# Optimization experiments

Measured on AMD Instinct MI355X. Metric: run time of the kernel, lower is better.

## Reference

```python
import jax, jax.numpy as jnp
import numpy as np

TEMP = 1.0

def setup_inputs() -> dict:
    key = jax.random.key(0)
    k1, k2 = jax.random.split(key)
    B, T, C, Vp1 = 16, 2048, 256, 1025
    z = jax.random.normal(k1, (B, T, C), dtype=jnp.float32)
    mask = jnp.ones((B, T, 1), dtype=jnp.float32)
    codebook_weight = jax.random.normal(k2, (Vp1, C), dtype=jnp.float32)
    return {"z": z, "mask": mask, "codebook_weight": codebook_weight}

def reference(z, mask, codebook_weight):
    # e = codebook.embedding.weight.clone().detach()[1:, :]
    e = jax.lax.stop_gradient(codebook_weight[1:, :])  # [V, C]
    b, t, c = z.shape
    V = e.shape[0]
    z_flat = z.reshape(-1, c)                          # [N, C], N = b*t
    # sim(): cosine-sim matmul + log_softmax + argmax one-hot quantize
    cos_sim = jnp.matmul(z_flat, e.T)                  # [N, V]
    log_probs = jax.nn.log_softmax(cos_sim / TEMP, axis=1)
    indices = jnp.argmax(log_probs, axis=1)            # [N]
    # one_hot @ e is exactly a row gather -- avoid materializing one_hot
    z_q = e[indices]                                   # [N, C]
    z_q3 = z_q.reshape(b, t, c)
    # loss(): masked commitment + smoothness
    valid_count = mask.sum() * c
    commitment_loss = (jnp.square(z - jax.lax.stop_gradient(z_q3)) * mask).sum() / valid_count
    smoothness_loss = (jnp.square(z[:, :-1, :] - z[:, 1:, :]) * mask[:, 1:, :]).sum() / valid_count
    # codebook_usage(): (one_hot * mask).sum(0) / mask.sum(), normalized
    mflat = mask.reshape(-1)                           # [N]
    prob = jax.ops.segment_sum(mflat, indices, num_segments=V) / mflat.sum()
    e_mean = prob / prob.sum()
    return (smoothness_loss, commitment_loss, log_probs.reshape(b, t, V), z_q3, e_mean)
```

## Files before the change

kernel.cpp:

```cpp
#include <hip/hip_runtime.h>
#include <hip/hip_bf16.h>

#define TPB 1024
#define BM 32
#define NROW 32768
#define NBLK (NROW / BM)
#define VV 1024
#define KD 256
#define TT 2048

#define LP_OFF 2L
#define ZQ_OFF (2L + 33554432L)
#define EM_OFF (33554434L + 8388608L)

#define WS_HIST 0
#define WS_CSUM 1024
#define WS_SSUM 2048
#define WS_MSUM 3072
#define WS_E8 4096
#define WS_NEED (4096 * 4 + 32 * 1024 * 8 * 2)

typedef __attribute__((ext_vector_type(8))) short bf16x8;
typedef __attribute__((ext_vector_type(4))) float f32x4;

__device__ __forceinline__ void gl_lds16(const float* g, float* l) {
  __builtin_amdgcn_global_load_lds(
      (const __attribute__((address_space(1))) void*)g,
      (__attribute__((address_space(3))) void*)l, 16, 0, 0);
}

__device__ __forceinline__ unsigned short f2bf(float x) {
  unsigned u = __float_as_uint(x);
  unsigned r = ((u >> 16) & 1u) + 0x7FFFu;
  return (unsigned short)((u + r) >> 16);
}

__device__ __forceinline__ unsigned foldf(float v) {
  unsigned b = __float_as_uint(v);
  return b ^ ((unsigned)((int)b >> 31) | 0x80000000u);
}
__device__ __forceinline__ float unfoldf(unsigned k) {
  unsigned s = (unsigned)((int)k >> 31);
  return __uint_as_float(k ^ (0x80000000u | (~s & 0x7FFFFFFFu)));
}

__global__ __launch_bounds__(256) void tok_prep(
    const float* __restrict__ cw, unsigned short* __restrict__ e8) {
  int t = blockIdx.x * 256 + threadIdx.x;
  int o = t >> 10, n = t & 1023;
  const float* src = cw + (size_t)(1 + n) * KD + (o << 3);
  float4 a = *(const float4*)src;
  float4 b = *(const float4*)(src + 4);
  int4 pk;
  pk.x = f2bf(a.x) | ((unsigned)f2bf(a.y) << 16);
  pk.y = f2bf(a.z) | ((unsigned)f2bf(a.w) << 16);
  pk.z = f2bf(b.x) | ((unsigned)f2bf(b.y) << 16);
  pk.w = f2bf(b.z) | ((unsigned)f2bf(b.w) << 16);
  int U = ((n >> 6) << 11) + ((o >> 2) << 8) + (((n >> 4) & 3) << 6) +
          ((o & 3) << 4) + (n & 15);
  *(int4*)(e8 + ((size_t)U << 3)) = pk;
}

__global__ __launch_bounds__(TPB, 4) void tok_mfma(
    const float* __restrict__ z, const float* __restrict__ mask,
    const float* __restrict__ cw, const unsigned short* __restrict__ e8,
    float* __restrict__ out, float* __restrict__ ws) {
  __shared__ __align__(16) float z_s[BM][260];
  __shared__ __align__(16) unsigned short z8u[8192];
  __shared__ unsigned wkey[16][2][33];
  __shared__ float wsum_s[16][33];
  __shared__ float Mrow_s[32], lse_s[32];
  __shared__ float exv_s[32][4];
  __shared__ int exi_s[32][4];
  __shared__ int argi[32];
  __shared__ float mask_s[32];
  __shared__ float cred[16], sred[16];

  const int tid = threadIdx.x;
  const int lane = tid & 63;
  const int w = tid >> 6;
  const int g = lane >> 4;
  const int lm = lane & 15;
  const int c0 = w << 6;
  const int n0 = blockIdx.x * BM;

  gl_lds16(&z[(size_t)(n0 + w) * KD + (lane << 2)], &z_s[w][0]);
  gl_lds16(&z[(size_t)(n0 + 16 + w) * KD + (lane << 2)], &z_s[16 + w][0]);
  if (tid < 32) mask_s[tid] = mask[n0 + tid];
  __syncthreads();

  {
    int r = tid >> 5, o = tid & 31;
    float4 a = *(const float4*)&z_s[r][o << 3];
    float4 b = *(const float4*)&z_s[r][(o << 3) + 4];
    int4 pk;
    pk.x = f2bf(a.x) | ((unsigned)f2bf(a.y) << 16);
    pk.y = f2bf(a.z) | ((unsigned)f2bf(a.w) << 16);
    pk.z = f2bf(b.x) | ((unsigned)f2bf(b.y) << 16);
    pk.w = f2bf(b.z) | ((unsigned)f2bf(b.w) << 16);
    *(int4*)&z8u[(unsigned)(((o << 5) + (r ^ ((o & 7) << 2))) << 3)] = pk;
  }
  __syncthreads();

  const bf16x8* za = (const bf16x8*)z8u;
  const bf16x8* bb = (const bf16x8*)e8 + (w << 11) + (g << 4) + lm;
  f32x4 accA[4], accB[4];
  const f32x4 zz = {0.f, 0.f, 0.f, 0.f};
#pragma unroll
  for (int nt = 0; nt < 4; ++nt) { accA[nt] = zz; accB[nt] = zz; }
  bf16x8 bA[4], bB[4], bC[4];
#pragma unroll
  for (int nt = 0; nt < 4; ++nt) bA[nt] = bb[nt << 6];
#pragma unroll
  for (int nt = 0; nt < 4; ++nt) bB[nt] = bb[256 + (nt << 6)];
#pragma unroll
  for (int step = 0; step < 8; ++step) {
    if (step < 6) {
#pragma unroll
      for (int nt = 0; nt < 4; ++nt) bC[nt] = bb[((step + 2) << 8) + (nt << 6)];
    }
    const int oct = (step << 2) + g;
    const int sw = (oct & 7) << 2;
    bf16x8 a0 = za[(oct << 5) + (lm ^ sw)];
    bf16x8 a1 = za[(oct << 5) + ((16 + lm) ^ sw)];
#pragma unroll
    for (int nt = 0; nt < 4; ++nt) {
      accA[nt] = __builtin_amdgcn_mfma_f32_16x16x32_bf16(a0, bA[nt], accA[nt], 0, 0, 0);
      accB[nt] = __builtin_amdgcn_mfma_f32_16x16x32_bf16(a1, bA[nt], accB[nt], 0, 0, 0);
    }
#pragma unroll
    for (int nt = 0; nt < 4; ++nt) { bA[nt] = bB[nt]; bB[nt] = bC[nt]; }
  }

  unsigned colpack[4];
#pragma unroll
  for (int nt = 0; nt < 4; ++nt)
    colpack[nt] = 1023u - (unsigned)(c0 + (nt << 4) + lm);

  auto phase1 = [&](f32x4(&ac)[4], int mt) {
#pragma unroll
    for (int j = 0; j < 4; ++j) {
      int r = (mt << 4) + (g << 2) + j;
      unsigned cur[4];
#pragma unroll
      for (int nt = 0; nt < 4; ++nt)
        cur[nt] = (foldf(ac[nt][j]) & 0xFFFFFC00u) | colpack[nt];
      unsigned k1 = cur[0];
#pragma unroll
      for (int nt = 1; nt < 4; ++nt) k1 = k1 > cur[nt] ? k1 : cur[nt];
#pragma unroll
      for (int d = 1; d <= 8; d <<= 1) {
        unsigned o2 = __shfl_xor(k1, d);
        k1 = k1 > o2 ? k1 : o2;
      }
#pragma unroll
      for (int nt = 0; nt < 4; ++nt)
        if (cur[nt] == k1) cur[nt] = 0u;
      unsigned k2 = cur[0];
#pragma unroll
      for (int nt = 1; nt < 4; ++nt) k2 = k2 > cur[nt] ? k2 : cur[nt];
#pragma unroll
      for (int d = 1; d <= 8; d <<= 1) {
        unsigned o2 = __shfl_xor(k2, d);
        k2 = k2 > o2 ? k2 : o2;
      }
      if (lm == 0) {
        wkey[w][0][r] = k1;
        wkey[w][1][r] = k2;
      }
    }
  };
  phase1(accA, 0);
  phase1(accB, 1);
  __syncthreads();

  if (tid < 32) {
    int r = tid;
    unsigned mk = wkey[0][0][r];
#pragma unroll
    for (int w2 = 1; w2 < 16; ++w2) {
      unsigned k = wkey[w2][0][r];
      mk = mk > k ? mk : k;
    }
    Mrow_s[r] = unfoldf(mk & 0xFFFFFC00u);
  }
  __syncthreads();

  auto phase2 = [&](f32x4(&ac)[4], int mt) {
#pragma unroll
    for (int j = 0; j < 4; ++j) {
      int r = (mt << 4) + (g << 2) + j;
      float M = Mrow_s[r];
      float s = 0.f;
#pragma unroll
      for (int nt = 0; nt < 4; ++nt) s += __expf(ac[nt][j] - M);
#pragma unroll
      for (int d = 1; d <= 8; d <<= 1) s += __shfl_xor(s, d);
      if (lm == 0) wsum_s[w][r] = s;
    }
  };
  phase2(accA, 0);
  phase2(accB, 1);
  __syncthreads();

  if (tid < 32) {
    int r = tid;
    float S = 0.f;
#pragma unroll
    for (int w2 = 0; w2 < 16; ++w2) S += wsum_s[w2][r];
    lse_s[r] = Mrow_s[r] + __logf(S);
  }
  __syncthreads();

  auto phase3 = [&](f32x4(&ac)[4], int mt) {
#pragma unroll
    for (int j = 0; j < 4; ++j) {
      int r = (mt << 4) + (g << 2) + j;
      float lse = lse_s[r];
      size_t base = LP_OFF + (size_t)(n0 + r) * VV;
#pragma unroll
      for (int nt = 0; nt < 4; ++nt)
        out[base + c0 + (nt << 4) + lm] = ac[nt][j] - lse;
    }
  };
  phase3(accA, 0);
  phase3(accB, 1);

#pragma unroll
  for (int rr = 0; rr < 2; ++rr) {
    int row = (w << 1) + rr;
    unsigned key = (lane < 32) ? wkey[lane >> 1][lane & 1][row] : 0u;
#pragma unroll
    for (int t2 = 0; t2 < 4; ++t2) {
      unsigned mk = key;
#pragma unroll
      for (int d = 1; d <= 32; d <<= 1) {
        unsigned o2 = __shfl_xor(mk, d);
        mk = mk > o2 ? mk : o2;
      }
      if (lane == 0) exi_s[row][t2] = (int)(1023u - (mk & 0x3FFu));
      if (key == mk) key = 0u;
    }
  }
  __syncthreads();

  {
    int p = lane >> 3;
    int seg = lane & 7;
    int row = (w << 1) + (p >> 2);
    int cd = p & 3;
    int cand = exi_s[row][cd];
    const float* er = cw + (size_t)(1 + cand) * KD + (seg << 5);
    const float* zr = &z_s[row][seg << 5];
    float s = 0.f;
#pragma unroll
    for (int i2 = 0; i2 < 8; ++i2) {
      float4 a4 = *(const float4*)(zr + (i2 << 2));
      float4 b4 = *(const float4*)(er + (i2 << 2));
      s += a4.x * b4.x + a4.y * b4.y + a4.z * b4.z + a4.w * b4.w;
    }
    s += __shfl_xor(s, 1);
    s += __shfl_xor(s, 2);
    s += __shfl_xor(s, 4);
    if (seg == 0) exv_s[row][cd] = s;
  }
  __syncthreads();

  if (tid < 32) {
    int row = tid;
    float bv = exv_s[row][0];
    int bi = exi_s[row][0];
#pragma unroll
    for (int c = 1; c < 4; ++c) {
      float v = exv_s[row][c];
      int ci = exi_s[row][c];
      if (v > bv || (v == bv && ci < bi)) { bv = v; bi = ci; }
    }
    argi[row] = bi;
    atomicAdd(&ws[WS_HIST + bi], mask_s[row]);
  }
  __syncthreads();

  float csum = 0.f, ssum = 0.f;
  const bool has_prev = (n0 % TT) != 0;
#pragma unroll
  for (int i = 0; i < 2; ++i) {
    int q = i * TPB + tid;
    int r = q >> 6;
    int c4 = (q & 63) << 2;
    int idx = argi[r];
    const float4 ev = *(const float4*)&cw[(size_t)(1 + idx) * KD + c4];
    const float4 zv = *(const float4*)&z_s[r][c4];
    *(float4*)&out[ZQ_OFF + (size_t)(n0 + r) * KD + c4] = ev;
    float mk = mask_s[r];
    float dx = zv.x - ev.x, dy = zv.y - ev.y, dz2 = zv.z - ev.z,
          dw = zv.w - ev.w;
    csum += mk * (dx * dx + dy * dy + dz2 * dz2 + dw * dw);
    if (r > 0) {
      const float4 pv = *(const float4*)&z_s[r - 1][c4];
      float ax = zv.x - pv.x, ay = zv.y - pv.y, az = zv.z - pv.z,
            aw = zv.w - pv.w;
      ssum += mk * (ax * ax + ay * ay + az * az + aw * aw);
    } else if (has_prev) {
      const float4 pv = *(const float4*)&z[(size_t)(n0 - 1) * KD + c4];
      float ax = zv.x - pv.x, ay = zv.y - pv.y, az = zv.z - pv.z,
            aw = zv.w - pv.w;
      ssum += mk * (ax * ax + ay * ay + az * az + aw * aw);
    }
  }
#pragma unroll
  for (int d = 1; d <= 32; d <<= 1) {
    csum += __shfl_xor(csum, d);
    ssum += __shfl_xor(ssum, d);
  }
  if (lane == 0) { cred[w] = csum; sred[w] = ssum; }
  __syncthreads();
  if (tid == 0) {
    float cs = 0.f, ss2 = 0.f;
#pragma unroll
    for (int i = 0; i < 16; ++i) { cs += cred[i]; ss2 += sred[i]; }
    ws[WS_CSUM + blockIdx.x] = cs;
    ws[WS_SSUM + blockIdx.x] = ss2;
    float ms = 0.f;
    for (int r2 = 0; r2 < BM; ++r2) ms += mask_s[r2];
    ws[WS_MSUM + blockIdx.x] = ms;
  }
}

__global__ __launch_bounds__(256, 2) void tok_fb(
    const float* __restrict__ z, const float* __restrict__ mask,
    const float* __restrict__ cw, float* __restrict__ out,
    float* __restrict__ ws) {
  __shared__ __align__(16) float z_s[BM][KD];
  __shared__ int argi_s[BM];
  __shared__ float cred[4], sred[4];
  const int tid = threadIdx.x;
  const int lane = tid & 63;
  const int wave = tid >> 6;
  const int n0 = blockIdx.x * BM;
  const float* e = cw + KD;
#pragma unroll
  for (int i = 0; i < 8; ++i) {
    int seg = wave * 8 + i;
    gl_lds16(&z[(size_t)(n0 + seg) * KD + lane * 4], &z_s[seg][0]);
  }
  __syncthreads();
  float acc[8][16];
#pragma unroll
  for (int r = 0; r < 8; ++r)
#pragma unroll
    for (int m = 0; m < 16; ++m) acc[r][m] = 0.f;
#pragma unroll 1
  for (int i = 0; i < 64; ++i) {
    float4 ef[16];
#pragma unroll
    for (int m = 0; m < 16; ++m)
      ef[m] = *(const float4*)&e[(size_t)((m << 6) + lane) * KD + (i << 2)];
    float4 zf[8];
#pragma unroll
    for (int rr = 0; rr < 8; ++rr)
      zf[rr] = *(const float4*)&z_s[(wave << 3) + rr][i << 2];
#pragma unroll
    for (int m = 0; m < 16; ++m)
#pragma unroll
      for (int rr = 0; rr < 8; ++rr)
        acc[rr][m] += zf[rr].x * ef[m].x + zf[rr].y * ef[m].y +
                      zf[rr].z * ef[m].z + zf[rr].w * ef[m].w;
  }
  const int rowbase = wave << 3;
#pragma unroll
  for (int rr = 0; rr < 8; ++rr) {
    float mv = acc[rr][0];
    int mc = lane;
#pragma unroll
    for (int m = 1; m < 16; ++m) {
      float v = acc[rr][m];
      int c = (m << 6) + lane;
      bool tk = v > mv;
      mc = tk ? c : mc;
      mv = tk ? v : mv;
    }
#pragma unroll
    for (int d = 32; d >= 1; d >>= 1) {
      float ov = __shfl_xor(mv, d);
      int oc = __shfl_xor(mc, d);
      bool tk = (ov > mv) || (ov == mv && oc < mc);
      mv = tk ? ov : mv;
      mc = tk ? oc : mc;
    }
    float sum = 0.f;
#pragma unroll
    for (int m = 0; m < 16; ++m) sum += __expf(acc[rr][m] - mv);
#pragma unroll
    for (int d = 32; d >= 1; d >>= 1) sum += __shfl_xor(sum, d);
    float lse = mv + __logf(sum);
    size_t base = LP_OFF + (size_t)(n0 + rowbase + rr) * VV;
#pragma unroll
    for (int m = 0; m < 16; ++m) out[base + (m << 6) + lane] = acc[rr][m] - lse;
    if (lane == 0) {
      argi_s[rowbase + rr] = mc;
      atomicAdd(&ws[WS_HIST + mc], mask[n0 + rowbase + rr]);
    }
  }
  __syncthreads();
  float csum = 0.f, ssum = 0.f;
  const bool has_prev = (n0 % TT) != 0;
#pragma unroll
  for (int i = 0; i < 8; ++i) {
    int q = i * 256 + tid;
    int r = q >> 6;
    int c4 = (q & 63) << 2;
    int idx = argi_s[r];
    const float4 ev = *(const float4*)&e[(size_t)idx * KD + c4];
    const float4 zv = *(const float4*)&z_s[r][c4];
    *(float4*)&out[ZQ_OFF + (size_t)(n0 + r) * KD + c4] = ev;
    float mk = mask[n0 + r];
    float dx = zv.x - ev.x, dy = zv.y - ev.y, dz2 = zv.z - ev.z, dw = zv.w - ev.w;
    csum += mk * (dx * dx + dy * dy + dz2 * dz2 + dw * dw);
    if (r > 0) {
      const float4 pv = *(const float4*)&z_s[r - 1][c4];
      float ax = zv.x - pv.x, ay = zv.y - pv.y, az = zv.z - pv.z, aw = zv.w - pv.w;
      ssum += mk * (ax * ax + ay * ay + az * az + aw * aw);
    } else if (has_prev) {
      const float4 pv = *(const float4*)&z[(size_t)(n0 - 1) * KD + c4];
      float ax = zv.x - pv.x, ay = zv.y - pv.y, az = zv.z - pv.z, aw = zv.w - pv.w;
      ssum += mk * (ax * ax + ay * ay + az * az + aw * aw);
    }
  }
#pragma unroll
  for (int d = 32; d >= 1; d >>= 1) {
    csum += __shfl_xor(csum, d);
    ssum += __shfl_xor(ssum, d);
  }
  if (lane == 0) { cred[wave] = csum; sred[wave] = ssum; }
  __syncthreads();
  if (tid == 0) {
    ws[WS_CSUM + blockIdx.x] = cred[0] + cred[1] + cred[2] + cred[3];
    ws[WS_SSUM + blockIdx.x] = sred[0] + sred[1] + sred[2] + sred[3];
    float ms = 0.f;
    for (int r2 = 0; r2 < BM; ++r2) ms += mask[n0 + r2];
    ws[WS_MSUM + blockIdx.x] = ms;
  }
}

__global__ __launch_bounds__(1024) void tok_final(const float* __restrict__ ws,
                                                  float* __restrict__ out) {
  const int t = threadIdx.x;
  const int lane = t & 63, w = t >> 6;
  __shared__ float red[16];
  auto blockReduce = [&](float v) -> float {
#pragma unroll
    for (int d = 32; d >= 1; d >>= 1) v += __shfl_xor(v, d);
    __syncthreads();
    if (lane == 0) red[w] = v;
    __syncthreads();
    float s = 0.f;
#pragma unroll
    for (int i = 0; i < 16; ++i) s += red[i];
    return s;
  };
  float Mtot = blockReduce(ws[WS_MSUM + t]);
  float Ctot = blockReduce(ws[WS_CSUM + t]);
  float Stot = blockReduce(ws[WS_SSUM + t]);
  float prob = ws[WS_HIST + t] / Mtot;
  float psum = blockReduce(prob);
  out[EM_OFF + t] = prob / psum;
  if (t == 0) {
    float vc = Mtot * (float)KD;
    out[0] = Stot / vc;
    out[1] = Ctot / vc;
  }
}

extern "C" void kernel_launch(void* const* d_in, const int* in_sizes, int n_in,
                              void* d_out, int out_size, void* d_ws,
                              size_t ws_size, hipStream_t stream) {
  const float* z = (const float*)d_in[0];
  const float* mask = (const float*)d_in[1];
  const float* cw = (const float*)d_in[2];
  float* out = (float*)d_out;
  float* ws = (float*)d_ws;
  hipMemsetAsync(ws, 0, 1024 * sizeof(float), stream);
  if (ws_size >= (size_t)WS_NEED) {
    unsigned short* e8 = (unsigned short*)(ws + WS_E8);
    tok_prep<<<128, 256, 0, stream>>>(cw, e8);
    tok_mfma<<<NBLK, TPB, 0, stream>>>(z, mask, cw, e8, out, ws);
  } else {
    tok_fb<<<NBLK, 256, 0, stream>>>(z, mask, cw, out, ws);
  }
  tok_final<<<1, 1024, 0, stream>>>(ws, out);
}
```

Measured before the change: 123.2 us.

## Halve waves per block, widen per-wave tile, pre-pack z to bf16 globally

Blocks drop from 16 to 8 waves, and each wave now covers 128 codebook columns with 8 accumulator tiles. z is converted to bf16 once in the prep kernel and written to a global workspace that the MFMA kernel reads directly, so the in-kernel LDS conversion goes away when the workspace is large enough. The separate max pass and sum pass are merged into one online pass that rescales per-wave partial sums, and the top-4 candidate selection moves into a single-thread insertion sort. Global stores are deferred to the end of the kernel, which raises register pressure and adds an extra global round trip for z (32 MB written, then read back).

```diff
diff --git a/kernel.cpp b/kernel.cpp
--- a/kernel.cpp
+++ b/kernel.cpp
@@ -1,7 +1,7 @@
 #include <hip/hip_runtime.h>
 #include <hip/hip_bf16.h>
 
-#define TPB 1024
+#define TPB 512
 #define BM 32
 #define NROW 32768
 #define NBLK (NROW / BM)
@@ -18,7 +18,9 @@
 #define WS_SSUM 2048
 #define WS_MSUM 3072
 #define WS_E8 4096
-#define WS_NEED (4096 * 4 + 32 * 1024 * 8 * 2)
+#define WS_Z8G (4096 + 131072)
+#define WS_NEED_E ((size_t)WS_Z8G * 4)
+#define WS_NEED_Z ((size_t)WS_Z8G * 4 + (size_t)NROW * KD * 2)
 
 typedef __attribute__((ext_vector_type(8))) short bf16x8;
 typedef __attribute__((ext_vector_type(4))) float f32x4;
@@ -44,121 +46,152 @@
   return __uint_as_float(k ^ (0x80000000u | (~s & 0x7FFFFFFFu)));
 }
 
-__global__ __launch_bounds__(256) void tok_prep(
-    const float* __restrict__ cw, unsigned short* __restrict__ e8) {
-  int t = blockIdx.x * 256 + threadIdx.x;
-  int o = t >> 10, n = t & 1023;
-  const float* src = cw + (size_t)(1 + n) * KD + (o << 3);
-  float4 a = *(const float4*)src;
-  float4 b = *(const float4*)(src + 4);
+__device__ __forceinline__ int4 pack8(const float* p) {
+  float4 a = *(const float4*)p;
+  float4 b = *(const float4*)(p + 4);
   int4 pk;
   pk.x = f2bf(a.x) | ((unsigned)f2bf(a.y) << 16);
   pk.y = f2bf(a.z) | ((unsigned)f2bf(a.w) << 16);
   pk.z = f2bf(b.x) | ((unsigned)f2bf(b.y) << 16);
   pk.w = f2bf(b.z) | ((unsigned)f2bf(b.w) << 16);
-  int U = ((n >> 6) << 11) + ((o >> 2) << 8) + (((n >> 4) & 3) << 6) +
+  return pk;
+}
+
+__global__ __launch_bounds__(256) void tok_prep(
+    const float* __restrict__ z, const float* __restrict__ cw,
+    unsigned short* __restrict__ e8, unsigned short* __restrict__ z8g,
+    int do_z) {
+  int t = blockIdx.x * 256 + threadIdx.x;
+  if (do_z && t < 1048576) {
+    int blk = t >> 10, oct = (t >> 5) & 31, row = t & 31;
+    *(int4*)(z8g + ((size_t)t << 3)) =
+        pack8(z + ((size_t)((blk << 5) + row) << 8) + (oct << 3));
+    return;
+  }
+  int t2 = do_z ? t - 1048576 : t;
+  if (t2 >= 32768) return;
+  int o = t2 >> 10, n = t2 & 1023;
+  int U = ((n >> 7) << 12) + ((o >> 2) << 9) + (((n >> 4) & 7) << 6) +
           ((o & 3) << 4) + (n & 15);
-  *(int4*)(e8 + ((size_t)U << 3)) = pk;
-}
-
-__global__ __launch_bounds__(TPB, 4) void tok_mfma(
+  *(int4*)(e8 + ((size_t)U << 3)) =
+      pack8(cw + ((size_t)(1 + n) << 8) + (o << 3));
+}
+
+template <int MODE>
+__global__ __launch_bounds__(TPB, 2) void tok_mfma(
     const float* __restrict__ z, const float* __restrict__ mask,
     const float* __restrict__ cw, const unsigned short* __restrict__ e8,
-    float* __restrict__ out, float* __restrict__ ws) {
-  __shared__ __align__(16) float z_s[BM][260];
-  __shared__ __align__(16) unsigned short z8u[8192];
-  __shared__ unsigned wkey[16][2][33];
-  __shared__ float wsum_s[16][33];
-  __shared__ float Mrow_s[32], lse_s[32];
-  __shared__ float exv_s[32][4];
-  __shared__ int exi_s[32][4];
-  __shared__ int argi[32];
-  __shared__ float mask_s[32];
-  __shared__ float cred[16], sred[16];
+    const unsigned short* __restrict__ z8g, float* __restrict__ out,
+    float* __restrict__ ws) {
+  __shared__ __align__(16) float z_s[BM][KD + 1];
+  __shared__ __align__(16) unsigned char upool[MODE == 1 ? 16384 : 4608];
+  __shared__ float mask_s[BM];
+  unsigned(*wkey)[2][33] = (unsigned(*)[2][33])upool;
+  float(*wsum)[33] = (float(*)[33])(upool + 2112);
+  float* lse_s = (float*)(upool + 3168);
+  float(*exv_s)[4] = (float(*)[4])(upool + 3296);
+  int(*exi_s)[4] = (int(*)[4])(upool + 3808);
+  int* argi = (int*)(upool + 4320);
+  float* cred = (float*)(upool + 4448);
+  float* sred = (float*)(upool + 4480);
 
   const int tid = threadIdx.x;
   const int lane = tid & 63;
   const int w = tid >> 6;
   const int g = lane >> 4;
   const int lm = lane & 15;
-  const int c0 = w << 6;
+  const int c0 = w << 7;
   const int n0 = blockIdx.x * BM;
 
-  gl_lds16(&z[(size_t)(n0 + w) * KD + (lane << 2)], &z_s[w][0]);
-  gl_lds16(&z[(size_t)(n0 + 16 + w) * KD + (lane << 2)], &z_s[16 + w][0]);
-  if (tid < 32) mask_s[tid] = mask[n0 + tid];
-  __syncthreads();
-
-  {
-    int r = tid >> 5, o = tid & 31;
-    float4 a = *(const float4*)&z_s[r][o << 3];
-    float4 b = *(const float4*)&z_s[r][(o << 3) + 4];
-    int4 pk;
-    pk.x = f2bf(a.x) | ((unsigned)f2bf(a.y) << 16);
-    pk.y = f2bf(a.z) | ((unsigned)f2bf(a.w) << 16);
-    pk.z = f2bf(b.x) | ((unsigned)f2bf(b.y) << 16);
-    pk.w = f2bf(b.z) | ((unsigned)f2bf(b.w) << 16);
-    *(int4*)&z8u[(unsigned)(((o << 5) + (r ^ ((o & 7) << 2))) << 3)] = pk;
-  }
-  __syncthreads();
-
-  const bf16x8* za = (const bf16x8*)z8u;
-  const bf16x8* bb = (const bf16x8*)e8 + (w << 11) + (g << 4) + lm;
-  f32x4 accA[4], accB[4];
+#pragma unroll
+  for (int i = 0; i < 4; ++i) {
+    int row = (w << 2) + i;
+    gl_lds16(&z[(size_t)(n0 + row) * KD + (lane << 2)], &z_s[row][0]);
+  }
+  if (tid < BM) mask_s[tid] = mask[n0 + tid];
+
+  if constexpr (MODE == 1) {
+    __syncthreads();
+#pragma unroll
+    for (int i = 0; i < 2; ++i) {
+      int c = (i << 9) + tid;
+      int oct = c >> 5, row = c & 31;
+      *(int4*)&upool[((oct << 5) + row) << 4] = pack8(&z_s[row][oct << 3]);
+    }
+    __syncthreads();
+  }
+
+  const bf16x8* Ap = (MODE == 2)
+                         ? ((const bf16x8*)z8g + ((size_t)blockIdx.x << 10))
+                         : (const bf16x8*)upool;
+  const bf16x8* Bp = (const bf16x8*)e8 + ((w << 12) + (g << 4) + lm);
+  f32x4 accA[8], accB[8];
   const f32x4 zz = {0.f, 0.f, 0.f, 0.f};
 #pragma unroll
-  for (int nt = 0; nt < 4; ++nt) { accA[nt] = zz; accB[nt] = zz; }
-  bf16x8 bA[4], bB[4], bC[4];
-#pragma unroll
-  for (int nt = 0; nt < 4; ++nt) bA[nt] = bb[nt << 6];
-#pragma unroll
-  for (int nt = 0; nt < 4; ++nt) bB[nt] = bb[256 + (nt << 6)];
-#pragma unroll
-  for (int step = 0; step < 8; ++step) {
-    if (step < 6) {
-#pragma unroll
-      for (int nt = 0; nt < 4; ++nt) bC[nt] = bb[((step + 2) << 8) + (nt << 6)];
-    }
-    const int oct = (step << 2) + g;
-    const int sw = (oct & 7) << 2;
-    bf16x8 a0 = za[(oct << 5) + (lm ^ sw)];
-    bf16x8 a1 = za[(oct << 5) + ((16 + lm) ^ sw)];
-#pragma unroll
-    for (int nt = 0; nt < 4; ++nt) {
-      accA[nt] = __builtin_amdgcn_mfma_f32_16x16x32_bf16(a0, bA[nt], accA[nt], 0, 0, 0);
-      accB[nt] = __builtin_amdgcn_mfma_f32_16x16x32_bf16(a1, bA[nt], accB[nt], 0, 0, 0);
-    }
-#pragma unroll
-    for (int nt = 0; nt < 4; ++nt) { bA[nt] = bB[nt]; bB[nt] = bC[nt]; }
-  }
-
-  unsigned colpack[4];
-#pragma unroll
-  for (int nt = 0; nt < 4; ++nt)
+  for (int nt = 0; nt < 8; ++nt) { accA[nt] = zz; accB[nt] = zz; }
+  bf16x8 Br[3][8];
+  bf16x8 Ar[3][2];
+#pragma unroll
+  for (int p = 0; p < 2; ++p) {
+#pragma unroll
+    for (int nt = 0; nt < 8; ++nt) Br[p][nt] = Bp[(p << 9) + (nt << 6)];
+    Ar[p][0] = Ap[(((p << 2) + g) << 5) + lm];
+    Ar[p][1] = Ap[(((p << 2) + g) << 5) + 16 + lm];
+  }
+#pragma unroll
+  for (int s = 0; s < 8; ++s) {
+    const int cs = s % 3, ns = (s + 2) % 3;
+    if (s < 6) {
+#pragma unroll
+      for (int nt = 0; nt < 8; ++nt)
+        Br[ns][nt] = Bp[((s + 2) << 9) + (nt << 6)];
+      Ar[ns][0] = Ap[((((s + 2) << 2) + g) << 5) + lm];
+      Ar[ns][1] = Ap[((((s + 2) << 2) + g) << 5) + 16 + lm];
+    }
+#pragma unroll
+    for (int nt = 0; nt < 8; ++nt) {
+      accA[nt] =
+          __builtin_amdgcn_mfma_f32_16x16x32_bf16(Ar[cs][0], Br[cs][nt], accA[nt], 0, 0, 0);
+      accB[nt] =
+          __builtin_amdgcn_mfma_f32_16x16x32_bf16(Ar[cs][1], Br[cs][nt], accB[nt], 0, 0, 0);
+    }
+  }
+
+  if constexpr (MODE == 1) __syncthreads();
+
+  unsigned colpack[8];
+#pragma unroll
+  for (int nt = 0; nt < 8; ++nt)
     colpack[nt] = 1023u - (unsigned)(c0 + (nt << 4) + lm);
 
-  auto phase1 = [&](f32x4(&ac)[4], int mt) {
+  auto phase1 = [&](f32x4(&ac)[8], int mt) {
 #pragma unroll
     for (int j = 0; j < 4; ++j) {
-      int r = (mt << 4) + (g << 2) + j;
-      unsigned cur[4];
-#pragma unroll
-      for (int nt = 0; nt < 4; ++nt)
+      const int r = (mt << 4) + (g << 2) + j;
+      unsigned cur[8];
+#pragma unroll
+      for (int nt = 0; nt < 8; ++nt)
         cur[nt] = (foldf(ac[nt][j]) & 0xFFFFFC00u) | colpack[nt];
       unsigned k1 = cur[0];
 #pragma unroll
-      for (int nt = 1; nt < 4; ++nt) k1 = k1 > cur[nt] ? k1 : cur[nt];
+      for (int nt = 1; nt < 8; ++nt) k1 = k1 > cur[nt] ? k1 : cur[nt];
 #pragma unroll
       for (int d = 1; d <= 8; d <<= 1) {
         unsigned o2 = __shfl_xor(k1, d);
         k1 = k1 > o2 ? k1 : o2;
       }
-#pragma unroll
-      for (int nt = 0; nt < 4; ++nt)
+      const float mw = unfoldf(k1 & 0xFFFFFC00u);
+      float sum = 0.f;
+#pragma unroll
+      for (int nt = 0; nt < 8; ++nt) sum += __expf(ac[nt][j] - mw);
+#pragma unroll
+      for (int d = 1; d <= 8; d <<= 1) sum += __shfl_xor(sum, d);
+#pragma unroll
+      for (int nt = 0; nt < 8; ++nt)
         if (cur[nt] == k1) cur[nt] = 0u;
       unsigned k2 = cur[0];
 #pragma unroll
-      for (int nt = 1; nt < 4; ++nt) k2 = k2 > cur[nt] ? k2 : cur[nt];
+      for (int nt = 1; nt < 8; ++nt) k2 = k2 > cur[nt] ? k2 : cur[nt];
 #pragma unroll
       for (int d = 1; d <= 8; d <<= 1) {
         unsigned o2 = __shfl_xor(k2, d);
@@ -167,6 +200,7 @@
       if (lm == 0) {
         wkey[w][0][r] = k1;
         wkey[w][1][r] = k2;
+        wsum[w][r] = sum;
       }
     }
   };
@@ -175,99 +209,54 @@
   __syncthreads();
 
   if (tid < 32) {
-    int r = tid;
-    unsigned mk = wkey[0][0][r];
-#pragma unroll
-    for (int w2 = 1; w2 < 16; ++w2) {
-      unsigned k = wkey[w2][0][r];
-      mk = mk > k ? mk : k;
-    }
-    Mrow_s[r] = unfoldf(mk & 0xFFFFFC00u);
-  }
-  __syncthreads();
-
-  auto phase2 = [&](f32x4(&ac)[4], int mt) {
-#pragma unroll
-    for (int j = 0; j < 4; ++j) {
-      int r = (mt << 4) + (g << 2) + j;
-      float M = Mrow_s[r];
-      float s = 0.f;
-#pragma unroll
-      for (int nt = 0; nt < 4; ++nt) s += __expf(ac[nt][j] - M);
-#pragma unroll
-      for (int d = 1; d <= 8; d <<= 1) s += __shfl_xor(s, d);
-      if (lm == 0) wsum_s[w][r] = s;
-    }
-  };
-  phase2(accA, 0);
-  phase2(accB, 1);
-  __syncthreads();
-
-  if (tid < 32) {
-    int r = tid;
+    const int r = tid;
+    unsigned best[4] = {0u, 0u, 0u, 0u};
+#pragma unroll
+    for (int w2 = 0; w2 < 8; ++w2)
+#pragma unroll
+      for (int k = 0; k < 2; ++k) {
+        unsigned x = wkey[w2][k][r];
+#pragma unroll
+        for (int q = 0; q < 4; ++q) {
+          unsigned mx = x > best[q] ? x : best[q];
+          unsigned mn = x > best[q] ? best[q] : x;
+          best[q] = mx;
+          x = mn;
+        }
+      }
+    const float M = unfoldf(best[0] & 0xFFFFFC00u);
     float S = 0.f;
 #pragma unroll
-    for (int w2 = 0; w2 < 16; ++w2) S += wsum_s[w2][r];
-    lse_s[r] = Mrow_s[r] + __logf(S);
-  }
-  __syncthreads();
-
-  auto phase3 = [&](f32x4(&ac)[4], int mt) {
-#pragma unroll
-    for (int j = 0; j < 4; ++j) {
-      int r = (mt << 4) + (g << 2) + j;
-      float lse = lse_s[r];
-      size_t base = LP_OFF + (size_t)(n0 + r) * VV;
-#pragma unroll
-      for (int nt = 0; nt < 4; ++nt)
-        out[base + c0 + (nt << 4) + lm] = ac[nt][j] - lse;
-    }
-  };
-  phase3(accA, 0);
-  phase3(accB, 1);
-
-#pragma unroll
-  for (int rr = 0; rr < 2; ++rr) {
-    int row = (w << 1) + rr;
-    unsigned key = (lane < 32) ? wkey[lane >> 1][lane & 1][row] : 0u;
-#pragma unroll
-    for (int t2 = 0; t2 < 4; ++t2) {
-      unsigned mk = key;
-#pragma unroll
-      for (int d = 1; d <= 32; d <<= 1) {
-        unsigned o2 = __shfl_xor(mk, d);
-        mk = mk > o2 ? mk : o2;
-      }
-      if (lane == 0) exi_s[row][t2] = (int)(1023u - (mk & 0x3FFu));
-      if (key == mk) key = 0u;
-    }
+    for (int w2 = 0; w2 < 8; ++w2)
+      S += wsum[w2][r] * __expf(unfoldf(wkey[w2][0][r] & 0xFFFFFC00u) - M);
+    lse_s[r] = M + __logf(S);
+#pragma unroll
+    for (int q = 0; q < 4; ++q) exi_s[r][q] = (int)(1023u - (best[q] & 0x3FFu));
   }
   __syncthreads();
 
   {
-    int p = lane >> 3;
-    int seg = lane & 7;
-    int row = (w << 1) + (p >> 2);
-    int cd = p & 3;
-    int cand = exi_s[row][cd];
-    const float* er = cw + (size_t)(1 + cand) * KD + (seg << 5);
-    const float* zr = &z_s[row][seg << 5];
+    const int row = (w << 2) + (lane >> 4);
+    const int cd = (lane >> 2) & 3;
+    const int seg = lane & 3;
+    const int cand = exi_s[row][cd];
+    const float* er = cw + (size_t)(1 + cand) * KD + (seg << 6);
+    const float* zr = &z_s[row][seg << 6];
     float s = 0.f;
 #pragma unroll
-    for (int i2 = 0; i2 < 8; ++i2) {
+    for (int i2 = 0; i2 < 16; ++i2) {
       float4 a4 = *(const float4*)(zr + (i2 << 2));
       float4 b4 = *(const float4*)(er + (i2 << 2));
       s += a4.x * b4.x + a4.y * b4.y + a4.z * b4.z + a4.w * b4.w;
     }
     s += __shfl_xor(s, 1);
     s += __shfl_xor(s, 2);
-    s += __shfl_xor(s, 4);
     if (seg == 0) exv_s[row][cd] = s;
   }
   __syncthreads();
 
   if (tid < 32) {
-    int row = tid;
+    const int row = tid;
     float bv = exv_s[row][0];
     int bi = exi_s[row][0];
 #pragma unroll
@@ -282,17 +271,17 @@
   __syncthreads();
 
   float csum = 0.f, ssum = 0.f;
+  float4 evs[4];
   const bool has_prev = (n0 % TT) != 0;
 #pragma unroll
-  for (int i = 0; i < 2; ++i) {
-    int q = i * TPB + tid;
-    int r = q >> 6;
-    int c4 = (q & 63) << 2;
-    int idx = argi[r];
+  for (int i = 0; i < 4; ++i) {
+    const int r = (i << 3) + w;
+    const int c4 = lane << 2;
+    const int idx = argi[r];
     const float4 ev = *(const float4*)&cw[(size_t)(1 + idx) * KD + c4];
+    evs[i] = ev;
     const float4 zv = *(const float4*)&z_s[r][c4];
-    *(float4*)&out[ZQ_OFF + (size_t)(n0 + r) * KD + c4] = ev;
-    float mk = mask_s[r];
+    const float mk = mask_s[r];
     float dx = zv.x - ev.x, dy = zv.y - ev.y, dz2 = zv.z - ev.z,
           dw = zv.w - ev.w;
     csum += mk * (dx * dx + dy * dy + dz2 * dz2 + dw * dw);
@@ -318,13 +307,32 @@
   if (tid == 0) {
     float cs = 0.f, ss2 = 0.f;
 #pragma unroll
-    for (int i = 0; i < 16; ++i) { cs += cred[i]; ss2 += sred[i]; }
+    for (int i = 0; i < 8; ++i) { cs += cred[i]; ss2 += sred[i]; }
     ws[WS_CSUM + blockIdx.x] = cs;
     ws[WS_SSUM + blockIdx.x] = ss2;
     float ms = 0.f;
     for (int r2 = 0; r2 < BM; ++r2) ms += mask_s[r2];
     ws[WS_MSUM + blockIdx.x] = ms;
   }
+
+#pragma unroll
+  for (int i = 0; i < 4; ++i) {
+    const int r = (i << 3) + w;
+    *(float4*)&out[ZQ_OFF + (size_t)(n0 + r) * KD + (lane << 2)] = evs[i];
+  }
+  auto phase3 = [&](f32x4(&ac)[8], int mt) {
+#pragma unroll
+    for (int j = 0; j < 4; ++j) {
+      const int r = (mt << 4) + (g << 2) + j;
+      const float lse = lse_s[r];
+      size_t base = LP_OFF + (size_t)(n0 + r) * VV;
+#pragma unroll
+      for (int nt = 0; nt < 8; ++nt)
+        out[base + c0 + (nt << 4) + lm] = ac[nt][j] - lse;
+    }
+  };
+  phase3(accA, 0);
+  phase3(accB, 1);
 }
 
 __global__ __launch_bounds__(256, 2) void tok_fb(
@@ -481,10 +489,14 @@
   float* out = (float*)d_out;
   float* ws = (float*)d_ws;
   hipMemsetAsync(ws, 0, 1024 * sizeof(float), stream);
-  if (ws_size >= (size_t)WS_NEED) {
-    unsigned short* e8 = (unsigned short*)(ws + WS_E8);
-    tok_prep<<<128, 256, 0, stream>>>(cw, e8);
-    tok_mfma<<<NBLK, TPB, 0, stream>>>(z, mask, cw, e8, out, ws);
+  unsigned short* e8 = (unsigned short*)(ws + WS_E8);
+  unsigned short* z8g = (unsigned short*)(ws + WS_Z8G);
+  if (ws_size >= WS_NEED_Z) {
+    tok_prep<<<4224, 256, 0, stream>>>(z, cw, e8, z8g, 1);
+    tok_mfma<2><<<NBLK, TPB, 0, stream>>>(z, mask, cw, e8, z8g, out, ws);
+  } else if (ws_size >= WS_NEED_E) {
+    tok_prep<<<128, 256, 0, stream>>>(z, cw, e8, nullptr, 0);
+    tok_mfma<1><<<NBLK, TPB, 0, stream>>>(z, mask, cw, e8, nullptr, out, ws);
   } else {
     tok_fb<<<NBLK, 256, 0, stream>>>(z, mask, cw, out, ws);
   }
```

After: 157.1 us. 1.27x slower.
